# Kernel optimization log

Measured on AMD Instinct MI355X. Metric: run time of the kernel, lower is better.

## Reference

```python
import jax, jax.numpy as jnp
import numpy as np

B, NP, NJ, ND = 16, 64, 15, 128
SIGMA = 15.0        # cfg.MULTI_PERSON.POSE_SIGMA
BIG = 1.0e5         # sentinel used to mask padded reference persons
EPS = 1e-8


def setup_inputs() -> dict:
    key = jax.random.key(0)
    k1, k2, k3, k4, k5 = jax.random.split(key, 5)
    # 3D plane-sweep hypotheses in the reference camera frame (z>0 so projection is safe)
    uv = jax.random.uniform(k1, (B, NP, NJ, ND, 2), minval=-0.5, maxval=0.5)
    z = jax.random.uniform(k2, (B, NP, NJ, ND, 1), minval=2.0, maxval=10.0)
    poses_3d = jnp.concatenate([uv * z, z], axis=-1).astype(jnp.float32)
    # detected 2D poses in the reference view, pixel coordinates
    poses_2d_ref = (jax.random.uniform(k3, (B, NP, NJ, 2)) * jnp.array([1920.0, 1080.0], jnp.float32)).astype(jnp.float32)
    vis_ref = (jax.random.uniform(k4, (B, NP, NJ)) < 0.8).astype(jnp.float32)
    num_persons_ref = jax.random.randint(k5, (B,), 1, NP + 1).astype(jnp.int32)
    R = jnp.tile(jnp.eye(3, dtype=jnp.float32), (B, 1, 1))
    T = jnp.zeros((B, 3), jnp.float32)
    f = jnp.full((B, 2), 1000.0, jnp.float32)
    c = jnp.tile(jnp.array([960.0, 540.0], jnp.float32), (B, 1))
    image_w = jnp.full((B,), 1920.0, jnp.float32)
    image_h = jnp.full((B,), 1080.0, jnp.float32)
    return dict(poses_3d=poses_3d, poses_2d_ref=poses_2d_ref, vis_ref=vis_ref,
                num_persons_ref=num_persons_ref, R=R, T=T, f=f, c=c,
                image_w=image_w, image_h=image_h)


def _project(pts, R, T, f, c):
    # pinhole projection: x_cam = R (X - T); 2d = f * xy/z + c
    xc = jnp.einsum('bij,bpkdj->bpkdi', R, pts - T[:, None, None, None, :])
    z = xc[..., 2:3]
    return f[:, None, None, None, :] * xc[..., :2] / z + c[:, None, None, None, :]


def reference(poses_3d, poses_2d_ref, vis_ref, num_persons_ref, R, T, f, c, image_w, image_h):
    # 1) project 3D hypotheses to the reference view -> [B,NP,NJ,ND,2]
    p2t = _project(poses_3d, R, T, f, c)
    # 2) visibility-weighted mean pairwise squared distance, expanded as
    #    |a|^2 + |b|^2 - 2 a.b to avoid the [B,NP,NP,NJ,ND,2] intermediate
    pt2 = jnp.sum(p2t ** 2, axis=-1)                      # [B,NP,NJ,ND]
    pr2 = jnp.sum(poses_2d_ref ** 2, axis=-1)             # [B,NQ,NJ]
    wpr = poses_2d_ref * vis_ref[..., None]               # [B,NQ,NJ,2]
    term1 = jnp.einsum('bpjd,bqj->bpqd', pt2, vis_ref)
    term2 = jnp.sum(pr2 * vis_ref, axis=-1)               # [B,NQ]
    term3 = jnp.einsum('bpjdc,bqjc->bpqd', p2t, wpr)
    vsum = jnp.sum(vis_ref, axis=-1)                      # [B,NQ]
    dist = (term1 + term2[:, None, :, None] - 2.0 * term3) / (vsum[:, None, :, None] + EPS)
    # 3) mask padded reference persons, nearest-pose matching
    valid = jnp.arange(NP)[None, :] < num_persons_ref[:, None]   # [B,NQ]
    dist = jnp.where(valid[:, None, :, None], dist, BIG)
    mm = jnp.argmin(dist, axis=2)                          # [B,NP,ND]
    # 4) gather matched 2D poses / visibilities
    b_idx = jnp.arange(B)[:, None, None]
    matched = jnp.transpose(poses_2d_ref[b_idx, mm], (0, 1, 3, 2, 4))  # [B,NP,NJ,ND,2]
    mvis = jnp.transpose(vis_ref[b_idx, mm], (0, 1, 3, 2))             # [B,NP,NJ,ND]
    # 5) exp score (non-panoptic branch) and in-image bounding
    mdist = jnp.sum((p2t - matched) ** 2, axis=-1)
    score = jnp.exp(-mdist / (SIGMA ** 2))
    iw = image_w[:, None, None, None]
    ih = image_h[:, None, None, None]
    inb = ((p2t[..., 0] >= 0) & (p2t[..., 1] >= 0) &
           (p2t[..., 0] <= iw - 1) & (p2t[..., 1] <= ih - 1)).astype(score.dtype)
    bounding = inb * mvis
    return score * bounding
```

## Files before the change

kernel.cpp:

```cpp
#include <hip/hip_runtime.h>

#define NPERS 64
#define NJOINT 15
#define NDEPTH 128
#define BIGF 100000.0f
#define EPSF 1e-8f
#define INFF 3.0e38f

#define F4E(v, e) ((e) == 0 ? (v).x : (e) == 1 ? (v).y : (e) == 2 ? (v).z : (v).w)

__global__ __launch_bounds__(256, 4)
void pose_match_kernel(
    const float* __restrict__ poses_3d,
    const float* __restrict__ p2d,
    const float* __restrict__ vis,
    const int*   __restrict__ nper,
    const float* __restrict__ Rm,
    const float* __restrict__ Tm,
    const float* __restrict__ fm,
    const float* __restrict__ cm,
    const float* __restrict__ iw_,
    const float* __restrict__ ih_,
    float* __restrict__ out)
{
    const int b    = blockIdx.x >> 6;
    const int rem  = blockIdx.x & 63;
    const int pp   = rem >> 1;
    const int dh   = rem & 1;
    const int p0   = pp * 2;
    const int tid  = threadIdx.x;
    const int lane = tid & 63;
    const int d    = dh * 64 + lane;
    const int wvs  = __builtin_amdgcn_readfirstlane(tid >> 6);

    __shared__ float4 sq[NPERS][NJOINT];
    __shared__ float4 sco2[NJOINT][48];
    __shared__ float  sc_c[NPERS];
    __shared__ float  bvred[4][2][64];
    __shared__ int    bqred[4][2][64];

    for (int i = tid; i < NPERS * NJOINT; i += 256) {
        int q = i / NJOINT, j = i % NJOINT;
        float v  = vis[(b * NPERS + q) * NJOINT + j];
        float rx = p2d[((b * NPERS + q) * NJOINT + j) * 2 + 0];
        float ry = p2d[((b * NPERS + q) * NJOINT + j) * 2 + 1];
        sq[q][j] = make_float4(v, rx, ry, 0.0f);
    }
    __syncthreads();

    if (tid < NPERS) {
        const int q = tid;
        float vs = 0.0f, t2 = 0.0f;
        #pragma unroll
        for (int j = 0; j < NJOINT; ++j) {
            float4 s = sq[q][j];
            vs += s.x;
            t2 = fmaf(s.y * s.y + s.z * s.z, s.x, t2);
        }
        float inv = 1.0f / (vs + EPSF);
        #pragma unroll
        for (int j = 0; j < NJOINT; ++j) {
            float4 s = sq[q][j];
            float* row = (float*)&sco2[j][0];
            row[q * 3 + 0] = s.x * inv;
            row[q * 3 + 1] = 2.0f * s.x * s.y * inv;
            row[q * 3 + 2] = 2.0f * s.x * s.z * inv;
        }
        sc_c[q] = t2 * inv;
    }
    __syncthreads();

    const float R00 = Rm[b*9+0], R01 = Rm[b*9+1], R02 = Rm[b*9+2];
    const float R10 = Rm[b*9+3], R11 = Rm[b*9+4], R12 = Rm[b*9+5];
    const float R20 = Rm[b*9+6], R21 = Rm[b*9+7], R22 = Rm[b*9+8];
    const float T0 = Tm[b*3+0], T1 = Tm[b*3+1], T2 = Tm[b*3+2];
    const float fx = fm[b*2+0], fy = fm[b*2+1];
    const float cx = cm[b*2+0], cy = cm[b*2+1];
    const float iwm1 = iw_[b] - 1.0f;
    const float ihm1 = ih_[b] - 1.0f;
    const int   npv  = nper[b];

    const int q0  = wvs * 16;
    const int nvs = __builtin_amdgcn_readfirstlane(
                        min(max(npv - q0, 0), 16));

    const float* pA = poses_3d +
        ((size_t)(b * NPERS + p0    ) * NJOINT * NDEPTH + d) * 3;
    const float* pB = poses_3d +
        ((size_t)(b * NPERS + p0 + 1) * NJOINT * NDEPTH + d) * 3;

    float acc0[16], acc1[16];
    #pragma unroll
    for (int k = 0; k < 16; ++k) { acc0[k] = 0.0f; acc1[k] = 0.0f; }

    if (nvs > 0) {
        #pragma unroll 1
        for (int j = 0; j < NJOINT; ++j) {
            const int off = j * NDEPTH * 3;
            float X0, Y0, X1, Y1;
            {
                float a0 = pA[off + 0] - T0;
                float a1 = pA[off + 1] - T1;
                float a2 = pA[off + 2] - T2;
                float xc0 = R00 * a0 + R01 * a1 + R02 * a2;
                float xc1 = R10 * a0 + R11 * a1 + R12 * a2;
                float xc2 = R20 * a0 + R21 * a1 + R22 * a2;
                float r   = __builtin_amdgcn_rcpf(xc2);
                X0 = fmaf(fx * xc0, r, cx);
                Y0 = fmaf(fy * xc1, r, cy);
            }
            {
                float a0 = pB[off + 0] - T0;
                float a1 = pB[off + 1] - T1;
                float a2 = pB[off + 2] - T2;
                float xc0 = R00 * a0 + R01 * a1 + R02 * a2;
                float xc1 = R10 * a0 + R11 * a1 + R12 * a2;
                float xc2 = R20 * a0 + R21 * a1 + R22 * a2;
                float r   = __builtin_amdgcn_rcpf(xc2);
                X1 = fmaf(fx * xc0, r, cx);
                Y1 = fmaf(fy * xc1, r, cy);
            }

            #pragma unroll
            for (int g = 0; g < 4; ++g) {
                if (g * 4 < nvs) {
                    float4 r0 = sco2[j][wvs * 12 + g * 3 + 0];
                    float4 r1 = sco2[j][wvs * 12 + g * 3 + 1];
                    float4 r2 = sco2[j][wvs * 12 + g * 3 + 2];
#define ACC1(K, W, WX, WY)                                                    \
                    {                                                         \
                        float u;                                              \
                        u = fmaf((W), X0, -(WX));                             \
                        acc0[g * 4 + K] = fmaf(X0, u, acc0[g * 4 + K]);       \
                        u = fmaf((W), Y0, -(WY));                             \
                        acc0[g * 4 + K] = fmaf(Y0, u, acc0[g * 4 + K]);       \
                        u = fmaf((W), X1, -(WX));                             \
                        acc1[g * 4 + K] = fmaf(X1, u, acc1[g * 4 + K]);       \
                        u = fmaf((W), Y1, -(WY));                             \
                        acc1[g * 4 + K] = fmaf(Y1, u, acc1[g * 4 + K]);       \
                    }
                    ACC1(0, r0.x, r0.y, r0.z)
                    ACC1(1, r0.w, r1.x, r1.y)
                    ACC1(2, r1.z, r1.w, r2.x)
                    ACC1(3, r2.y, r2.z, r2.w)
#undef ACC1
                }
            }
        }
    }

    float bv0, bv1;
    int   bq0, bq1;
    if (npv < NPERS) { bv0 = bv1 = BIGF; bq0 = bq1 = npv; }
    else             { bv0 = bv1 = INFF; bq0 = bq1 = 0;   }
    #pragma unroll
    for (int k = 0; k < 16; ++k) {
        if (k < nvs) {
            float cterm = sc_c[q0 + k];
            float d0 = acc0[k] + cterm;
            float d1 = acc1[k] + cterm;
            if (d0 < bv0) { bv0 = d0; bq0 = q0 + k; }
            if (d1 < bv1) { bv1 = d1; bq1 = q0 + k; }
        }
    }
    bvred[wvs][0][lane] = bv0;  bqred[wvs][0][lane] = bq0;
    bvred[wvs][1][lane] = bv1;  bqred[wvs][1][lane] = bq1;
    __syncthreads();

#define EPILOGUE(PI, PPTR)                                                    \
    if (wvs == PI) {                                                          \
        float bestv = bvred[0][PI][lane];                                     \
        int   bestq = bqred[0][PI][lane];                                     \
        _Pragma("unroll")                                                     \
        for (int k = 1; k < 4; ++k) {                                         \
            float v  = bvred[k][PI][lane];                                    \
            int   qq = bqred[k][PI][lane];                                    \
            if (v < bestv || (v == bestv && qq < bestq)) {                    \
                bestv = v; bestq = qq;                                        \
            }                                                                 \
        }                                                                     \
        const int obase = ((b * NPERS + p0 + PI) * NJOINT) * NDEPTH + d;      \
        _Pragma("unroll")                                                     \
        for (int j = 0; j < NJOINT; ++j) {                                    \
            const int off = j * NDEPTH * 3;                                   \
            float a0 = PPTR[off + 0] - T0;                                    \
            float a1 = PPTR[off + 1] - T1;                                    \
            float a2 = PPTR[off + 2] - T2;                                    \
            float xc0 = R00 * a0 + R01 * a1 + R02 * a2;                       \
            float xc1 = R10 * a0 + R11 * a1 + R12 * a2;                       \
            float xc2 = R20 * a0 + R21 * a1 + R22 * a2;                       \
            float r   = __builtin_amdgcn_rcpf(xc2);                           \
            float xx  = fmaf(fx * xc0, r, cx);                                \
            float yy  = fmaf(fy * xc1, r, cy);                                \
            float4 v = sq[bestq][j];                                          \
            float dx = xx - v.y;                                              \
            float dy = yy - v.z;                                              \
            float md = fmaf(dx, dx, dy * dy);                                 \
            float sc = __expf(-md * (1.0f / 225.0f));                         \
            float inb = (xx >= 0.0f && yy >= 0.0f &&                          \
                         xx <= iwm1 && yy <= ihm1) ? 1.0f : 0.0f;             \
            out[obase + j * NDEPTH] = sc * inb * v.x;                         \
        }                                                                     \
    }

    EPILOGUE(0, pA)
    EPILOGUE(1, pB)
#undef EPILOGUE
}

extern "C" void kernel_launch(void* const* d_in, const int* in_sizes, int n_in,
                              void* d_out, int out_size, void* d_ws, size_t ws_size,
                              hipStream_t stream) {
    const float* poses_3d = (const float*)d_in[0];
    const float* p2d      = (const float*)d_in[1];
    const float* vis      = (const float*)d_in[2];
    const int*   nper     = (const int*)d_in[3];
    const float* Rm       = (const float*)d_in[4];
    const float* Tm       = (const float*)d_in[5];
    const float* fm       = (const float*)d_in[6];
    const float* cm       = (const float*)d_in[7];
    const float* iw       = (const float*)d_in[8];
    const float* ih       = (const float*)d_in[9];
    float* out = (float*)d_out;

    const int B = in_sizes[3];
    dim3 grid(B * 64);
    dim3 block(256);
    pose_match_kernel<<<grid, block, 0, stream>>>(
        poses_3d, p2d, vis, nper, Rm, Tm, fm, cm, iw, ih, out);
}
```

Measured before the change: 30.43 us.

## Project hypotheses once into shared memory and split work across waves

Each of the four waves now projects a disjoint subset of joints once and stores the 2D coordinates in LDS. Before, every wave redundantly loaded and projected all 15 joints, and the epilogue projected them again. The per-person coefficient setup moves to wave 3, running alongside the projection and removing one barrier. This cuts redundant global loads and ALU work, at the cost of extra LDS traffic and a 15 KB shared buffer that may reduce occupancy.

```diff
diff --git a/kernel.cpp b/kernel.cpp
--- a/kernel.cpp
+++ b/kernel.cpp
@@ -6,8 +6,6 @@
 #define BIGF 100000.0f
 #define EPSF 1e-8f
 #define INFF 3.0e38f
-
-#define F4E(v, e) ((e) == 0 ? (v).x : (e) == 1 ? (v).y : (e) == 2 ? (v).z : (v).w)
 
 __global__ __launch_bounds__(256, 4)
 void pose_match_kernel(
@@ -36,6 +34,7 @@
     __shared__ float4 sq[NPERS][NJOINT];
     __shared__ float4 sco2[NJOINT][48];
     __shared__ float  sc_c[NPERS];
+    __shared__ float4 sxy[NJOINT][64];
     __shared__ float  bvred[4][2][64];
     __shared__ int    bqred[4][2][64];
 
@@ -45,28 +44,6 @@
         float rx = p2d[((b * NPERS + q) * NJOINT + j) * 2 + 0];
         float ry = p2d[((b * NPERS + q) * NJOINT + j) * 2 + 1];
         sq[q][j] = make_float4(v, rx, ry, 0.0f);
-    }
-    __syncthreads();
-
-    if (tid < NPERS) {
-        const int q = tid;
-        float vs = 0.0f, t2 = 0.0f;
-        #pragma unroll
-        for (int j = 0; j < NJOINT; ++j) {
-            float4 s = sq[q][j];
-            vs += s.x;
-            t2 = fmaf(s.y * s.y + s.z * s.z, s.x, t2);
-        }
-        float inv = 1.0f / (vs + EPSF);
-        #pragma unroll
-        for (int j = 0; j < NJOINT; ++j) {
-            float4 s = sq[q][j];
-            float* row = (float*)&sco2[j][0];
-            row[q * 3 + 0] = s.x * inv;
-            row[q * 3 + 1] = 2.0f * s.x * s.y * inv;
-            row[q * 3 + 2] = 2.0f * s.x * s.z * inv;
-        }
-        sc_c[q] = t2 * inv;
     }
     __syncthreads();
 
@@ -80,22 +57,36 @@
     const float ihm1 = ih_[b] - 1.0f;
     const int   npv  = nper[b];
 
-    const int q0  = wvs * 16;
-    const int nvs = __builtin_amdgcn_readfirstlane(
-                        min(max(npv - q0, 0), 16));
-
     const float* pA = poses_3d +
         ((size_t)(b * NPERS + p0    ) * NJOINT * NDEPTH + d) * 3;
     const float* pB = poses_3d +
         ((size_t)(b * NPERS + p0 + 1) * NJOINT * NDEPTH + d) * 3;
 
-    float acc0[16], acc1[16];
+    if (wvs == 3) {
+        const int q = lane;
+        float vs = 0.0f, t2 = 0.0f;
+        #pragma unroll
+        for (int j = 0; j < NJOINT; ++j) {
+            float4 s = sq[q][j];
+            vs += s.x;
+            t2 = fmaf(s.y * s.y + s.z * s.z, s.x, t2);
+        }
+        float inv = 1.0f / (vs + EPSF);
+        #pragma unroll
+        for (int j = 0; j < NJOINT; ++j) {
+            float4 s = sq[q][j];
+            float* row = (float*)&sco2[j][0];
+            row[q * 3 + 0] = s.x * inv;
+            row[q * 3 + 1] = 2.0f * s.x * s.y * inv;
+            row[q * 3 + 2] = 2.0f * s.x * s.z * inv;
+        }
+        sc_c[q] = t2 * inv;
+    }
+
     #pragma unroll
-    for (int k = 0; k < 16; ++k) { acc0[k] = 0.0f; acc1[k] = 0.0f; }
-
-    if (nvs > 0) {
-        #pragma unroll 1
-        for (int j = 0; j < NJOINT; ++j) {
+    for (int jj = 0; jj < 4; ++jj) {
+        const int j = wvs + jj * 4;
+        if (j < NJOINT) {
             const int off = j * NDEPTH * 3;
             float X0, Y0, X1, Y1;
             {
@@ -120,6 +111,24 @@
                 X1 = fmaf(fx * xc0, r, cx);
                 Y1 = fmaf(fy * xc1, r, cy);
             }
+            sxy[j][lane] = make_float4(X0, Y0, X1, Y1);
+        }
+    }
+    __syncthreads();
+
+    const int q0  = wvs * 16;
+    const int nvs = __builtin_amdgcn_readfirstlane(
+                        min(max(npv - q0, 0), 16));
+
+    float acc0[16], acc1[16];
+    #pragma unroll
+    for (int k = 0; k < 16; ++k) { acc0[k] = 0.0f; acc1[k] = 0.0f; }
+
+    if (nvs > 0) {
+        #pragma unroll 1
+        for (int j = 0; j < NJOINT; ++j) {
+            float4 xy = sxy[j][lane];
+            const float X0 = xy.x, Y0 = xy.y, X1 = xy.z, Y1 = xy.w;
 
             #pragma unroll
             for (int g = 0; g < 4; ++g) {
@@ -167,7 +176,7 @@
     bvred[wvs][1][lane] = bv1;  bqred[wvs][1][lane] = bq1;
     __syncthreads();
 
-#define EPILOGUE(PI, PPTR)                                                    \
+#define EPILOGUE(PI)                                                          \
     if (wvs == PI) {                                                          \
         float bestv = bvred[0][PI][lane];                                     \
         int   bestq = bqred[0][PI][lane];                                     \
@@ -182,16 +191,9 @@
         const int obase = ((b * NPERS + p0 + PI) * NJOINT) * NDEPTH + d;      \
         _Pragma("unroll")                                                     \
         for (int j = 0; j < NJOINT; ++j) {                                    \
-            const int off = j * NDEPTH * 3;                                   \
-            float a0 = PPTR[off + 0] - T0;                                    \
-            float a1 = PPTR[off + 1] - T1;                                    \
-            float a2 = PPTR[off + 2] - T2;                                    \
-            float xc0 = R00 * a0 + R01 * a1 + R02 * a2;                       \
-            float xc1 = R10 * a0 + R11 * a1 + R12 * a2;                       \
-            float xc2 = R20 * a0 + R21 * a1 + R22 * a2;                       \
-            float r   = __builtin_amdgcn_rcpf(xc2);                           \
-            float xx  = fmaf(fx * xc0, r, cx);                                \
-            float yy  = fmaf(fy * xc1, r, cy);                                \
+            float4 xy = sxy[j][lane];                                         \
+            float xx = (PI == 0) ? xy.x : xy.z;                               \
+            float yy = (PI == 0) ? xy.y : xy.w;                               \
             float4 v = sq[bestq][j];                                          \
             float dx = xx - v.y;                                              \
             float dy = yy - v.z;                                              \
@@ -203,8 +205,8 @@
         }                                                                     \
     }
 
-    EPILOGUE(0, pA)
-    EPILOGUE(1, pB)
+    EPILOGUE(0)
+    EPILOGUE(1)
 #undef EPILOGUE
 }
 
```

Result: slower. 33.46 us (+10.0%).
